# Kernel optimization log

Hardware: AMD Instinct MI355X
Metric: run time of the kernel (lower is better)

## Reference

```python
import jax, jax.numpy as jnp
import numpy as np

EMB = 1024
H = 16
HD = EMB // H  # 64
TEMP = 8.0  # sqrt(head_dim)


def setup_inputs() -> dict:
    key = jax.random.key(0)
    ks = jax.random.split(key, 7)
    B, S = 2, 2048
    s = 1.0 / np.sqrt(EMB)
    return {
        "query": jax.random.normal(ks[0], (B, S, EMB), jnp.float32),
        "key": jax.random.normal(ks[1], (B, S, EMB), jnp.float32),
        "value": jax.random.normal(ks[2], (B, S, EMB), jnp.float32),
        "Wq": jax.random.normal(ks[3], (EMB, EMB), jnp.float32) * s,
        "Wk": jax.random.normal(ks[4], (EMB, EMB), jnp.float32) * s,
        "Wv": jax.random.normal(ks[5], (EMB, EMB), jnp.float32) * s,
        "Wo": jax.random.normal(ks[6], (EMB, EMB), jnp.float32) * s,
    }


def reference(query, key, value, Wq, Wk, Wv, Wo):
    B, S, _ = query.shape
    # linear projections (torch Linear: x @ W.T), then split heads -> [B,H,S,hd]
    def proj(x, W):
        return (x @ W.T).reshape(B, -1, H, HD).transpose(0, 2, 1, 3)
    q = proj(query, Wq)
    k = proj(key, Wk)
    v = proj(value, Wv)
    # scaled dot-product attention with explicit score matrix [B,H,S,S]
    scores = jnp.einsum("bhqd,bhkd->bhqk", q, k) / TEMP
    attn = jax.nn.softmax(scores, axis=-1)
    x = jnp.einsum("bhqk,bhkd->bhqd", attn, v)
    # concat heads and final linear
    x = x.transpose(0, 2, 1, 3).reshape(B, S, H * HD)
    return x @ Wo.T
```

## Files before the change

kernel.cpp:

```cpp
#include <hip/hip_runtime.h>
#include <hip/hip_bf16.h>
#include <stdint.h>

#define SEQ   2048
#define EMB_D 1024
#define NHEAD 16
#define HDIM  64
#define MROWS 4096
#define KDIM  1024

typedef __attribute__((ext_vector_type(8)))  short          short8;
typedef __attribute__((ext_vector_type(8)))  unsigned short ushort8;
typedef __attribute__((ext_vector_type(4)))  float          f32x4;
typedef __attribute__((ext_vector_type(16))) float          f32x16;

#define LOG2E 1.4426950408889634f
#define QSCALE (0.125f * LOG2E)

__device__ __forceinline__ unsigned short f2bf(float f) {
  union { float f; uint32_t u; } v; v.f = f;
  return (unsigned short)((v.u + 0x7fffu + ((v.u >> 16) & 1u)) >> 16);
}

__device__ __forceinline__ uint32_t packbf(float a, float b) {
  union { __hip_bfloat16 h; unsigned short u; } ca, cb;
  ca.h = __float2bfloat16(a); cb.h = __float2bfloat16(b);
  return (uint32_t)ca.u | ((uint32_t)cb.u << 16);
}

__device__ __forceinline__ void gload16(const void* g, void* l) {
  __builtin_amdgcn_global_load_lds((const __attribute__((address_space(1))) void*)g,
                                   (__attribute__((address_space(3))) void*)l,
                                   16, 0, 0);
}

__device__ __forceinline__ f32x4 mfma16(short8 a, short8 b, f32x4 c) {
  return __builtin_amdgcn_mfma_f32_16x16x32_bf16(a, b, c, 0, 0, 0);
}
__device__ __forceinline__ f32x16 mfma32(short8 a, short8 b, f32x16 c) {
  return __builtin_amdgcn_mfma_f32_32x32x16_bf16(a, b, c, 0, 0, 0);
}

__device__ __forceinline__ void cvt_body(const float* __restrict__ src,
                                         unsigned short* __restrict__ dst, int i) {
  const float4* s = (const float4*)src;
  float4 a = s[2 * i], b = s[2 * i + 1];
  ushort8 o;
  o[0] = f2bf(a.x); o[1] = f2bf(a.y); o[2] = f2bf(a.z); o[3] = f2bf(a.w);
  o[4] = f2bf(b.x); o[5] = f2bf(b.y); o[6] = f2bf(b.z); o[7] = f2bf(b.w);
  *((ushort8*)dst + i) = o;
}

__global__ void cvt3_kernel(const float* __restrict__ s0, const float* __restrict__ s1,
                            const float* __restrict__ s2,
                            unsigned short* __restrict__ d0, unsigned short* __restrict__ d1,
                            unsigned short* __restrict__ d2, int n8) {
  int i = blockIdx.x * blockDim.x + threadIdx.x;
  if (i >= n8) return;
  const float* s      = blockIdx.y == 0 ? s0 : blockIdx.y == 1 ? s1 : s2;
  unsigned short* d   = blockIdx.y == 0 ? d0 : blockIdx.y == 1 ? d1 : d2;
  cvt_body(s, d, i);
}

__global__ void cvt4_kernel(const float* __restrict__ s0, const float* __restrict__ s1,
                            const float* __restrict__ s2, const float* __restrict__ s3,
                            unsigned short* __restrict__ d0, unsigned short* __restrict__ d1,
                            unsigned short* __restrict__ d2, unsigned short* __restrict__ d3,
                            int n8) {
  int i = blockIdx.x * blockDim.x + threadIdx.x;
  if (i >= n8) return;
  const float* s    = blockIdx.y == 0 ? s0 : blockIdx.y == 1 ? s1 : blockIdx.y == 2 ? s2 : s3;
  unsigned short* d = blockIdx.y == 0 ? d0 : blockIdx.y == 1 ? d1 : blockIdx.y == 2 ? d2 : d3;
  cvt_body(s, d, i);
}

__device__ __forceinline__ void gemm_tile(const unsigned short* __restrict__ A,
                                          const unsigned short* __restrict__ Bw,
                                          unsigned short* lsA, unsigned short* lsB,
                                          int m0, int n0, f32x4 acc[4][4]) {
  const int tid  = threadIdx.x;
  const int lane = tid & 63;
  const int w    = tid >> 6;
  const int wr   = w >> 1;
  const int wc   = w & 1;
  const int lr   = lane & 15;
  const int lk8  = (lane >> 4) * 8;

  for (int k0 = 0; k0 < KDIM; k0 += 32) {
#pragma unroll
    for (int c = 0; c < 2; ++c) {
      int o   = c * 4096 + w * 1024;
      int oo  = o + lane * 16;
      int row = oo >> 6;
      int ce  = (oo & 63) >> 1;
      gload16(A  + (size_t)(m0 + row) * KDIM + k0 + ce, (char*)lsA + o);
      gload16(Bw + (size_t)(n0 + row) * KDIM + k0 + ce, (char*)lsB + o);
    }
    __syncthreads();

    short8 af[4], bf_[4];
#pragma unroll
    for (int m = 0; m < 4; ++m)
      af[m] = *(const short8*)(lsA + (wr * 64 + m * 16 + lr) * 32 + lk8);
#pragma unroll
    for (int n = 0; n < 4; ++n)
      bf_[n] = *(const short8*)(lsB + (wc * 64 + n * 16 + lr) * 32 + lk8);
#pragma unroll
    for (int m = 0; m < 4; ++m)
#pragma unroll
      for (int n = 0; n < 4; ++n)
        acc[m][n] = mfma16(af[m], bf_[n], acc[m][n]);
    __syncthreads();
  }
}

__global__ __launch_bounds__(256) void gemm_qkv(const unsigned short* __restrict__ Xq,
                                                const unsigned short* __restrict__ Xk,
                                                const unsigned short* __restrict__ Xv,
                                                const unsigned short* __restrict__ Wq,
                                                const unsigned short* __restrict__ Wk,
                                                const unsigned short* __restrict__ Wv,
                                                unsigned short* __restrict__ Qb,
                                                unsigned short* __restrict__ Kb,
                                                unsigned short* __restrict__ Vt) {
  __shared__ __align__(16) unsigned short lsA[128 * 32];
  __shared__ __align__(16) unsigned short lsB[128 * 32];
  const int z = blockIdx.z;
  const unsigned short* A  = z == 0 ? Xq : z == 1 ? Xk : Xv;
  const unsigned short* Bw = z == 0 ? Wq : z == 1 ? Wk : Wv;
  const int m0 = blockIdx.y * 128;
  const int n0 = blockIdx.x * 128;

  f32x4 acc[4][4] = {};
  gemm_tile(A, Bw, lsA, lsB, m0, n0, acc);

  const int lane = threadIdx.x & 63;
  const int w    = threadIdx.x >> 6;
  const int wr = w >> 1, wc = w & 1;
  const int crow = (lane >> 4) * 4;
  const int ccol = lane & 15;
#pragma unroll
  for (int m = 0; m < 4; ++m) {
#pragma unroll
    for (int n = 0; n < 4; ++n) {
#pragma unroll
      for (int r = 0; r < 4; ++r) {
        int row = m0 + wr * 64 + m * 16 + crow + r;
        int col = n0 + wc * 64 + n * 16 + ccol;
        float vv = acc[m][n][r];
        int b = row >> 11, s = row & 2047;
        int h = col >> 6,  d = col & 63;
        if (z == 0)
          Qb[((size_t)(b * NHEAD + h) * SEQ + s) * HDIM + d] = f2bf(vv * QSCALE);
        else if (z == 1)
          Kb[((size_t)(b * NHEAD + h) * SEQ + s) * HDIM + d] = f2bf(vv);
        else
          Vt[((size_t)(b * NHEAD + h) * HDIM + d) * SEQ + s] = f2bf(vv);
      }
    }
  }
}

__global__ __launch_bounds__(256) void gemm_out(const unsigned short* __restrict__ A,
                                                const unsigned short* __restrict__ Bw,
                                                float* __restrict__ Cout) {
  __shared__ __align__(16) unsigned short lsA[128 * 32];
  __shared__ __align__(16) unsigned short lsB[128 * 32];
  const int m0 = blockIdx.y * 128;
  const int n0 = blockIdx.x * 128;
  f32x4 acc[4][4] = {};
  gemm_tile(A, Bw, lsA, lsB, m0, n0, acc);

  const int lane = threadIdx.x & 63;
  const int w    = threadIdx.x >> 6;
  const int wr = w >> 1, wc = w & 1;
  const int crow = (lane >> 4) * 4;
  const int ccol = lane & 15;
#pragma unroll
  for (int m = 0; m < 4; ++m)
#pragma unroll
    for (int n = 0; n < 4; ++n)
#pragma unroll
      for (int r = 0; r < 4; ++r) {
        int row = m0 + wr * 64 + m * 16 + crow + r;
        int col = n0 + wc * 64 + n * 16 + ccol;
        Cout[(size_t)row * EMB_D + col] = acc[m][n][r];
      }
}

__device__ __forceinline__ void load_kv(const unsigned short* __restrict__ Kg,
                                        const unsigned short* __restrict__ Vg,
                                        int kv, int ln, int hi,
                                        short8 (&kf)[4], short8& v00, short8& v01,
                                        short8& v10, short8& v11) {
#pragma unroll
  for (int ds = 0; ds < 4; ++ds)
    kf[ds] = *(const short8*)(Kg + (size_t)(kv + ln) * HDIM + ds * 16 + hi * 8);
  v00 = *(const short8*)(Vg + (size_t)(ln)      * SEQ + kv +      hi * 8);
  v01 = *(const short8*)(Vg + (size_t)(ln)      * SEQ + kv + 16 + hi * 8);
  v10 = *(const short8*)(Vg + (size_t)(32 + ln) * SEQ + kv +      hi * 8);
  v11 = *(const short8*)(Vg + (size_t)(32 + ln) * SEQ + kv + 16 + hi * 8);
}

__device__ __forceinline__ void attn_tile(const short8 (&qf)[4], const short8 (&kf)[4],
                                          const short8& vf00, const short8& vf01,
                                          const short8& vf10, const short8& vf11,
                                          int hi, f32x16& o0, f32x16& o1, float& l) {
  f32x16 st = {};
#pragma unroll
  for (int ds = 0; ds < 4; ++ds) st = mfma32(kf[ds], qf[ds], st);

  float p[16];
  float rs = 0.f;
#pragma unroll
  for (int r = 0; r < 16; ++r) { p[r] = exp2f(st[r]); rs += p[r]; }
  rs += __shfl_xor(rs, 32);
  l += rs;

  uint32_t wv_[8], sw[8];
#pragma unroll
  for (int i = 0; i < 8; ++i) wv_[i] = packbf(p[2 * i], p[2 * i + 1]);
#pragma unroll
  for (int i = 0; i < 8; ++i) sw[i] = __shfl_xor(wv_[i], 32);

  union { uint32_t u[4]; short8 s; } pb0, pb1;
  pb0.u[0] = hi ? sw[2]  : wv_[0];
  pb0.u[1] = hi ? sw[3]  : wv_[1];
  pb0.u[2] = hi ? wv_[2] : sw[0];
  pb0.u[3] = hi ? wv_[3] : sw[1];
  pb1.u[0] = hi ? sw[6]  : wv_[4];
  pb1.u[1] = hi ? sw[7]  : wv_[5];
  pb1.u[2] = hi ? wv_[6] : sw[4];
  pb1.u[3] = hi ? wv_[7] : sw[5];

  f32x16 t0 = o0, t1 = o1;
  t0 = mfma32(vf00, pb0.s, t0);
  t0 = mfma32(vf01, pb1.s, t0);
  t1 = mfma32(vf10, pb0.s, t1);
  t1 = mfma32(vf11, pb1.s, t1);
  o0 = t0; o1 = t1;
}

__global__ __launch_bounds__(256) void attn_kernel(const unsigned short* __restrict__ Qb,
                                                   const unsigned short* __restrict__ Kb,
                                                   const unsigned short* __restrict__ Vt,
                                                   unsigned short* __restrict__ AO) {
  const int lane = threadIdx.x & 63;
  const int w    = threadIdx.x >> 6;
  const int xcd  = blockIdx.x & 7;
  const int slot = blockIdx.x >> 3;
  const int bh   = xcd + 8 * (slot >> 4);
  const int qt4  = slot & 15;
  const int b    = bh >> 4;
  const int h    = bh & 15;
  const unsigned short* Qg = Qb + (size_t)bh * SEQ * HDIM;
  const unsigned short* Kg = Kb + (size_t)bh * SEQ * HDIM;
  const unsigned short* Vg = Vt + (size_t)bh * HDIM * SEQ;

  const int ln = lane & 31;
  const int hi = lane >> 5;
  const int q0 = qt4 * 128 + w * 32;

  short8 qf[4];
#pragma unroll
  for (int ds = 0; ds < 4; ++ds)
    qf[ds] = *(const short8*)(Qg + (size_t)(q0 + ln) * HDIM + ds * 16 + hi * 8);

  f32x16 o0 = {}, o1 = {};
  float l = 0.f;

  short8 kA[4], kB[4];
  short8 vA00, vA01, vA10, vA11, vB00, vB01, vB10, vB11;

  load_kv(Kg, Vg, 0, ln, hi, kA, vA00, vA01, vA10, vA11);
  for (int kv = 0; kv < SEQ; kv += 64) {
    load_kv(Kg, Vg, kv + 32, ln, hi, kB, vB00, vB01, vB10, vB11);
    attn_tile(qf, kA, vA00, vA01, vA10, vA11, hi, o0, o1, l);
    int nkv = (kv + 64 < SEQ) ? kv + 64 : 0;
    load_kv(Kg, Vg, nkv, ln, hi, kA, vA00, vA01, vA10, vA11);
    attn_tile(qf, kB, vB00, vB01, vB10, vB11, hi, o0, o1, l);
  }

  float inv = 1.0f / l;
  unsigned short* orow = AO + ((size_t)b * SEQ + q0 + ln) * EMB_D + h * HDIM + hi * 4;
#pragma unroll
  for (int g = 0; g < 4; ++g) {
    uint2 d0, d1;
    d0.x = packbf(o0[4 * g + 0] * inv, o0[4 * g + 1] * inv);
    d0.y = packbf(o0[4 * g + 2] * inv, o0[4 * g + 3] * inv);
    d1.x = packbf(o1[4 * g + 0] * inv, o1[4 * g + 1] * inv);
    d1.y = packbf(o1[4 * g + 2] * inv, o1[4 * g + 3] * inv);
    *(uint2*)(orow + g * 8)      = d0;
    *(uint2*)(orow + 32 + g * 8) = d1;
  }
}

extern "C" void kernel_launch(void* const* d_in, const int* in_sizes, int n_in,
                              void* d_out, int out_size, void* d_ws, size_t ws_size,
                              hipStream_t stream) {
  const float* q  = (const float*)d_in[0];
  const float* k  = (const float*)d_in[1];
  const float* v  = (const float*)d_in[2];
  const float* wq = (const float*)d_in[3];
  const float* wk = (const float*)d_in[4];
  const float* wv = (const float*)d_in[5];
  const float* wo = (const float*)d_in[6];
  float* out = (float*)d_out;

  unsigned short* p = (unsigned short*)d_ws;
  unsigned short* Xq  = p; p += (size_t)MROWS * EMB_D;
  unsigned short* Xk  = p; p += (size_t)MROWS * EMB_D;
  unsigned short* Xv  = p; p += (size_t)MROWS * EMB_D;
  unsigned short* Wqb = p; p += (size_t)EMB_D * EMB_D;
  unsigned short* Wkb = p; p += (size_t)EMB_D * EMB_D;
  unsigned short* Wvb = p; p += (size_t)EMB_D * EMB_D;
  unsigned short* Wob = p; p += (size_t)EMB_D * EMB_D;
  unsigned short* Qb  = p; p += (size_t)MROWS * EMB_D;
  unsigned short* Kb  = p; p += (size_t)MROWS * EMB_D;
  unsigned short* Vt  = p; p += (size_t)MROWS * EMB_D;
  unsigned short* AO  = p; p += (size_t)MROWS * EMB_D;

  const int nx = MROWS * EMB_D / 8;
  const int nw = EMB_D * EMB_D / 8;
  dim3 g3((nx + 255) / 256, 3);
  cvt3_kernel<<<g3, 256, 0, stream>>>(q, k, v, Xq, Xk, Xv, nx);
  dim3 g4((nw + 255) / 256, 4);
  cvt4_kernel<<<g4, 256, 0, stream>>>(wq, wk, wv, wo, Wqb, Wkb, Wvb, Wob, nw);

  dim3 gq(EMB_D / 128, MROWS / 128, 3);
  gemm_qkv<<<gq, 256, 0, stream>>>(Xq, Xk, Xv, Wqb, Wkb, Wvb, Qb, Kb, Vt);

  attn_kernel<<<512, 256, 0, stream>>>(Qb, Kb, Vt, AO);

  dim3 gg(EMB_D / 128, MROWS / 128);
  gemm_out<<<gg, 256, 0, stream>>>(AO, Wob, out);
}
```

Before: 296.5 us.

## Stage K/V tiles through double-buffered swizzled LDS in attention kernel

Replaces per-wave direct global loads of K and V with block-cooperative staging into double-buffered shared memory. The tiles use an XOR swizzle and are loaded with a gload16 helper, presumably direct-to-LDS. All four waves now share one K/V tile instead of each fetching its own copy, which cuts global and L2 traffic. The cross-lane row-sum shuffle is also moved out of the inner loop to a single reduction at the end. In exchange the kernel adds LDS usage and a __syncthreads per 64-key tile, which may lower occupancy and add barrier stalls.

```diff
diff --git a/kernel.cpp b/kernel.cpp
--- a/kernel.cpp
+++ b/kernel.cpp
@@ -188,63 +188,13 @@
       }
 }
 
-__device__ __forceinline__ void load_kv(const unsigned short* __restrict__ Kg,
-                                        const unsigned short* __restrict__ Vg,
-                                        int kv, int ln, int hi,
-                                        short8 (&kf)[4], short8& v00, short8& v01,
-                                        short8& v10, short8& v11) {
-#pragma unroll
-  for (int ds = 0; ds < 4; ++ds)
-    kf[ds] = *(const short8*)(Kg + (size_t)(kv + ln) * HDIM + ds * 16 + hi * 8);
-  v00 = *(const short8*)(Vg + (size_t)(ln)      * SEQ + kv +      hi * 8);
-  v01 = *(const short8*)(Vg + (size_t)(ln)      * SEQ + kv + 16 + hi * 8);
-  v10 = *(const short8*)(Vg + (size_t)(32 + ln) * SEQ + kv +      hi * 8);
-  v11 = *(const short8*)(Vg + (size_t)(32 + ln) * SEQ + kv + 16 + hi * 8);
-}
-
-__device__ __forceinline__ void attn_tile(const short8 (&qf)[4], const short8 (&kf)[4],
-                                          const short8& vf00, const short8& vf01,
-                                          const short8& vf10, const short8& vf11,
-                                          int hi, f32x16& o0, f32x16& o1, float& l) {
-  f32x16 st = {};
-#pragma unroll
-  for (int ds = 0; ds < 4; ++ds) st = mfma32(kf[ds], qf[ds], st);
-
-  float p[16];
-  float rs = 0.f;
-#pragma unroll
-  for (int r = 0; r < 16; ++r) { p[r] = exp2f(st[r]); rs += p[r]; }
-  rs += __shfl_xor(rs, 32);
-  l += rs;
-
-  uint32_t wv_[8], sw[8];
-#pragma unroll
-  for (int i = 0; i < 8; ++i) wv_[i] = packbf(p[2 * i], p[2 * i + 1]);
-#pragma unroll
-  for (int i = 0; i < 8; ++i) sw[i] = __shfl_xor(wv_[i], 32);
-
-  union { uint32_t u[4]; short8 s; } pb0, pb1;
-  pb0.u[0] = hi ? sw[2]  : wv_[0];
-  pb0.u[1] = hi ? sw[3]  : wv_[1];
-  pb0.u[2] = hi ? wv_[2] : sw[0];
-  pb0.u[3] = hi ? wv_[3] : sw[1];
-  pb1.u[0] = hi ? sw[6]  : wv_[4];
-  pb1.u[1] = hi ? sw[7]  : wv_[5];
-  pb1.u[2] = hi ? wv_[6] : sw[4];
-  pb1.u[3] = hi ? wv_[7] : sw[5];
-
-  f32x16 t0 = o0, t1 = o1;
-  t0 = mfma32(vf00, pb0.s, t0);
-  t0 = mfma32(vf01, pb1.s, t0);
-  t1 = mfma32(vf10, pb0.s, t1);
-  t1 = mfma32(vf11, pb1.s, t1);
-  o0 = t0; o1 = t1;
-}
-
 __global__ __launch_bounds__(256) void attn_kernel(const unsigned short* __restrict__ Qb,
                                                    const unsigned short* __restrict__ Kb,
                                                    const unsigned short* __restrict__ Vt,
                                                    unsigned short* __restrict__ AO) {
+  __shared__ __align__(16) unsigned short lsK[2][64 * 64];
+  __shared__ __align__(16) unsigned short lsV[2][64 * 64];
+
   const int lane = threadIdx.x & 63;
   const int w    = threadIdx.x >> 6;
   const int xcd  = blockIdx.x & 7;
@@ -269,19 +219,77 @@
   f32x16 o0 = {}, o1 = {};
   float l = 0.f;
 
-  short8 kA[4], kB[4];
-  short8 vA00, vA01, vA10, vA11, vB00, vB01, vB10, vB11;
-
-  load_kv(Kg, Vg, 0, ln, hi, kA, vA00, vA01, vA10, vA11);
-  for (int kv = 0; kv < SEQ; kv += 64) {
-    load_kv(Kg, Vg, kv + 32, ln, hi, kB, vB00, vB01, vB10, vB11);
-    attn_tile(qf, kA, vA00, vA01, vA10, vA11, hi, o0, o1, l);
-    int nkv = (kv + 64 < SEQ) ? kv + 64 : 0;
-    load_kv(Kg, Vg, nkv, ln, hi, kA, vA00, vA01, vA10, vA11);
-    attn_tile(qf, kB, vB00, vB01, vB10, vB11, hi, o0, o1, l);
-  }
-
+  const int srow = (lane >> 3);
+  const int ssw8 = ((lane & 7) ^ srow) << 3;
+
+#define STAGE(T, C)                                                              \
+  {                                                                              \
+    int kv0_ = (T) * 64;                                                         \
+    _Pragma("unroll")                                                            \
+    for (int j = 0; j < 2; ++j) {                                                \
+      int row_ = w * 8 + j * 32 + srow;                                          \
+      gload16(Kg + (size_t)(kv0_ + row_) * HDIM + ssw8,                          \
+              &lsK[C][w * 512 + j * 2048 + lane * 8]);                           \
+      gload16(Vg + (size_t)row_ * SEQ + kv0_ + ssw8,                             \
+              &lsV[C][w * 512 + j * 2048 + lane * 8]);                           \
+    }                                                                            \
+  }
+
+  STAGE(0, 0);
+  __syncthreads();
+
+  const int l7 = ln & 7;
+  for (int t = 0; t < 32; ++t) {
+    const int cur = t & 1;
+    if (t + 1 < 32) STAGE(t + 1, cur ^ 1);
+
+#pragma unroll
+    for (int s = 0; s < 2; ++s) {
+      short8 kf[4];
+#pragma unroll
+      for (int ds = 0; ds < 4; ++ds)
+        kf[ds] = *(const short8*)&lsK[cur][(s * 32 + ln) * 64 + ((((ds << 1) | hi) ^ l7) << 3)];
+      short8 vf00 = *(const short8*)&lsV[cur][(ln)      * 64 + (((s * 4 + 0 + hi) ^ l7) << 3)];
+      short8 vf01 = *(const short8*)&lsV[cur][(ln)      * 64 + (((s * 4 + 2 + hi) ^ l7) << 3)];
+      short8 vf10 = *(const short8*)&lsV[cur][(32 + ln) * 64 + (((s * 4 + 0 + hi) ^ l7) << 3)];
+      short8 vf11 = *(const short8*)&lsV[cur][(32 + ln) * 64 + (((s * 4 + 2 + hi) ^ l7) << 3)];
+
+      f32x16 st = {};
+#pragma unroll
+      for (int ds = 0; ds < 4; ++ds) st = mfma32(kf[ds], qf[ds], st);
+
+      float p[16];
+#pragma unroll
+      for (int r = 0; r < 16; ++r) { p[r] = exp2f(st[r]); l += p[r]; }
+
+      uint32_t wv_[8], sw[8];
+#pragma unroll
+      for (int i = 0; i < 8; ++i) wv_[i] = packbf(p[2 * i], p[2 * i + 1]);
+#pragma unroll
+      for (int i = 0; i < 8; ++i) sw[i] = __shfl_xor(wv_[i], 32);
+
+      union { uint32_t u[4]; short8 s; } pb0, pb1;
+      pb0.u[0] = hi ? sw[2]  : wv_[0];
+      pb0.u[1] = hi ? sw[3]  : wv_[1];
+      pb0.u[2] = hi ? wv_[2] : sw[0];
+      pb0.u[3] = hi ? wv_[3] : sw[1];
+      pb1.u[0] = hi ? sw[6]  : wv_[4];
+      pb1.u[1] = hi ? sw[7]  : wv_[5];
+      pb1.u[2] = hi ? wv_[6] : sw[4];
+      pb1.u[3] = hi ? wv_[7] : sw[5];
+
+      o0 = mfma32(vf00, pb0.s, o0);
+      o0 = mfma32(vf01, pb1.s, o0);
+      o1 = mfma32(vf10, pb0.s, o1);
+      o1 = mfma32(vf11, pb1.s, o1);
+    }
+    __syncthreads();
+  }
+#undef STAGE
+
+  l += __shfl_xor(l, 32);
   float inv = 1.0f / l;
+
   unsigned short* orow = AO + ((size_t)b * SEQ + q0 + ln) * EMB_D + h * HDIM + hi * 4;
 #pragma unroll
   for (int g = 0; g < 4; ++g) {
```

Result: faster. 253.4 us (-14.5%).
